# Kernel tuning notes

Measured on AMD Instinct MI355X. Metric: run time of the kernel, lower is better.

The kernel has to match this reference:

```python
import jax, jax.numpy as jnp
import numpy as np

MAX_SCALE = 4
EPS = 1e-7        # tf.keras.backend.epsilon()
BN_EPS = 1e-3     # Keras BatchNormalization default epsilon


def setup_inputs() -> dict:
    key = jax.random.key(0)
    k1, = jax.random.split(key, 1)
    B, H, W, C = 16, 224, 224, 32
    x = jax.random.uniform(k1, (B, H, W, C), dtype=jnp.float32)
    gamma = jnp.ones((C,), jnp.float32)
    beta = jnp.zeros((C,), jnp.float32)
    moving_mean = jnp.zeros((C,), jnp.float32)
    moving_var = jnp.ones((C,), jnp.float32)
    return {"x": x, "gamma": gamma, "beta": beta,
            "moving_mean": moving_mean, "moving_var": moving_var}


def _box_sum(x, r):
    # Depthwise conv with an all-ones (r, r) kernel, SAME padding (NHWC).
    # reduce_window SAME padding matches TF conv SAME for stride 1.
    return jax.lax.reduce_window(x, 0.0, jax.lax.add,
                                 window_dimensions=(1, r, r, 1),
                                 window_strides=(1, 1, 1, 1),
                                 padding="SAME")


def reference(x, gamma, beta, moving_mean, moving_var):
    # sample_min_max_scaling: per-sample min-max over H, W, C
    mn = jnp.min(x, axis=(1, 2, 3), keepdims=True)
    mx = jnp.max(x, axis=(1, 2, 3), keepdims=True)
    xs = (x - mn) / (mx - mn + EPS)

    scales = [2 ** i for i in range(1, MAX_SCALE + 1)]  # [2,4,8,16]
    # measures: [B, H, W, C, S]
    measures = jnp.stack([_box_sum(xs, r) for r in scales], axis=-1)

    # OLS slope of log(measure) vs log(scale), per pixel/channel
    log_scales = jnp.log(jnp.asarray(scales, jnp.float32))        # [S]
    log_measures = jnp.log(measures + EPS)                         # [B,H,W,C,S]
    ls_c = log_scales - jnp.mean(log_scales)                       # centered [S]
    lm_c = log_measures - jnp.mean(log_measures, axis=-1, keepdims=True)
    alphas = jnp.sum(lm_c * ls_c, axis=-1) / jnp.sum(ls_c ** 2)    # [B,H,W,C]

    # BatchNorm, inference mode (training=False)
    inv = jax.lax.rsqrt(moving_var + BN_EPS)
    return (alphas - moving_mean) * inv * gamma + beta
```

## Files before the change

### kernel.cpp

```cpp
#include <hip/hip_runtime.h>
#include <cstdint>

#define B_ 16
#define H_ 224
#define W_ 224
#define C_ 32
#define HW_ (H_*W_)

__device__ __forceinline__ unsigned int enc_f32(float f) {
    unsigned int u = __float_as_uint(f);
    return (u & 0x80000000u) ? ~u : (u | 0x80000000u);
}
__device__ __forceinline__ float dec_f32(unsigned int u) {
    unsigned int v = (u & 0x80000000u) ? (u & 0x7fffffffu) : ~u;
    return __uint_as_float(v);
}

__global__ void k_init(unsigned int* scratch) {
    int t = threadIdx.x;
    if (t < B_) { scratch[t] = 0xFFFFFFFFu; scratch[B_ + t] = 0u; }
}

__global__ __launch_bounds__(256) void k_minmax(
        const float* __restrict__ x, unsigned int* __restrict__ scratch) {
    __shared__ float rmin[4], rmax[4];
    int t = threadIdx.x;
    int b = blockIdx.y;
    const float4* p = (const float4*)(x + (size_t)b * HW_ * C_);
    const int n4 = HW_ * C_ / 4;
    float vmin = 1e30f, vmax = -1e30f;
    for (int i = blockIdx.x * 256 + t; i < n4; i += gridDim.x * 256) {
        float4 v = p[i];
        vmin = fminf(vmin, fminf(fminf(v.x, v.y), fminf(v.z, v.w)));
        vmax = fmaxf(vmax, fmaxf(fmaxf(v.x, v.y), fmaxf(v.z, v.w)));
    }
    for (int off = 32; off; off >>= 1) {
        vmin = fminf(vmin, __shfl_down(vmin, off));
        vmax = fmaxf(vmax, __shfl_down(vmax, off));
    }
    if ((t & 63) == 0) { rmin[t >> 6] = vmin; rmax[t >> 6] = vmax; }
    __syncthreads();
    if (t == 0) {
        atomicMin(&scratch[b],      enc_f32(fminf(fminf(rmin[0], rmin[1]), fminf(rmin[2], rmin[3]))));
        atomicMax(&scratch[B_ + b], enc_f32(fmaxf(fmaxf(rmax[0], rmax[1]), fmaxf(rmax[2], rmax[3]))));
    }
}

__global__ __launch_bounds__(1024, 4) void k_fused(
        const float* __restrict__ x, float* __restrict__ out,
        const float* __restrict__ gamma, const float* __restrict__ beta,
        const float* __restrict__ mmean, const float* __restrict__ mvar,
        const unsigned int* __restrict__ scratch) {
    __shared__ float lin[2][16][132];
    __shared__ float lout[2][16][132];
    const int t    = threadIdx.x;
    const int wid  = t >> 6;
    const int lane = t & 63;

    int bid   = blockIdx.x;
    int cg    = bid & 1;
    int strip = (bid >> 1) & 1;
    int chunk = (bid >> 2) & 3;
    int b     = bid >> 4;

    const int cbase = cg * 16;
    const int c     = cbase + wid;
    const int h0    = chunk * 56;
    const int sbase = strip * 112;

    float sc = gamma[c] * rsqrtf(mvar[c] + 1e-3f);
    float bi = beta[c] - mmean[c] * sc;

    float mn   = dec_f32(scratch[b]);
    float mx   = dec_f32(scratch[B_ + b]);
    float inv  = 1.0f / (mx - mn + 1e-7f);
    float minv = mn * inv;

    int c0 = sbase - 8 + 2 * lane;
    int c1 = c0 + 1;
    bool mC = (c0 >= 0) && (c0 <= W_ - 2);

    int col_l = t >> 3;
    int lch   = (t & 7) * 2;
    int wld   = min(max(sbase - 8 + col_l, 0), W_ - 1);
    int wst   = sbase - 8 + col_l;
    bool colok = (col_l >= 8) && (col_l < 120);
    const float* xb = x   + (size_t)b * HW_ * C_ + cbase + lch;
    float*       ob = out + (size_t)b * HW_ * C_ + cbase + lch;

    float cw2_0  = (float)(min(c0+1, W_-1) - c0 + 1);
    float cw2_1  = (float)(min(c1+1, W_-1) - c1 + 1);
    float cw4_0  = (float)(min(c0+2, W_-1) - max(c0-1, 0) + 1);
    float cw4_1  = (float)(min(c1+2, W_-1) - max(c1-1, 0) + 1);
    float cw8_0  = (float)(min(c0+4, W_-1) - max(c0-3, 0) + 1);
    float cw8_1  = (float)(min(c1+4, W_-1) - max(c1-3, 0) + 1);
    float cw16_0 = (float)(min(c0+8, W_-1) - max(c0-7, 0) + 1);
    float cw16_1 = (float)(min(c1+8, W_-1) - max(c1-7, 0) + 1);
    float e2_0  = minv * cw2_0,  e2_1  = minv * cw2_1;
    float e4_0  = minv * cw4_0,  e4_1  = minv * cw4_1;
    float e8_0  = minv * cw8_0,  e8_1  = minv * cw8_1;
    float e16_0 = minv * cw16_0, e16_1 = minv * cw16_1;
    float d2_0  = 1e-7f -  2.0f * e2_0,  d2_1  = 1e-7f -  2.0f * e2_1;
    float d4_0  = 1e-7f -  4.0f * e4_0,  d4_1  = 1e-7f -  4.0f * e4_1;
    float d8_0  = 1e-7f -  8.0f * e8_0,  d8_1  = 1e-7f -  8.0f * e8_1;
    float d16_0 = 1e-7f - 16.0f * e16_0, d16_1 = 1e-7f - 16.0f * e16_1;

    float hp0 = 0.f, hp1 = 0.f;
    float rB4[2][2]  = {};
    float rB8[2][4]  = {};
    float rB16[2][8] = {};
    float acc[2][8]  = {};

#define LDROW(AR) (*(const float2*)(xb + (size_t)((min(max((AR), 0), H_-1)) * W_ + wld) * C_))

    float2 q0, q1;
    {
        float2 qi = LDROW(h0 - 7);
        lin[1][lch][col_l]     = qi.x;
        lin[1][lch + 1][col_l] = qi.y;
        q0 = LDROW(h0 - 6);
        q1 = LDROW(h0 - 5);
    }

    for (int g8 = 0; g8 < 9; ++g8) {
        #pragma unroll
        for (int u = 0; u < 8; ++u) {
            int it = g8 * 8 + u;
            int a  = h0 - 7 + it;
            __syncthreads();
            float2 lv = *(const float2*)&lin[(u + 1) & 1][wid][2 * lane];
            lin[u & 1][lch][col_l]     = q0.x;
            lin[u & 1][lch + 1][col_l] = q0.y;
            q0 = q1;
            q1 = LDROW(a + 3);
            if (it >= 16 && colok) {
                int op = h0 - 16 + it;
                float2 sv;
                sv.x = lout[u & 1][lch][col_l];
                sv.y = lout[u & 1][lch + 1][col_l];
                *(float2*)(ob + (size_t)(op * W_ + wst) * C_) = sv;
            }

            bool rowok = (a >= 0) && (a < H_);
            float x0 = (rowok && mC) ? lv.x : 0.f;
            float x1 = (rowok && mC) ? lv.y : 0.f;
            float nx0 = __shfl_down(x0, 1);
            float xh0 = x0 + x1;
            float xh1 = x1 + nx0;
            float g2_0 = hp0 + xh0; hp0 = xh0;
            float g2_1 = hp1 + xh1; hp1 = xh1;
            float b4n_0 = g2_0 + __shfl_down(g2_0, 1);
            float b4n_1 = g2_1 + __shfl_down(g2_1, 1);
            float a4_0 = rB4[0][u & 1] + b4n_0; rB4[0][u & 1] = b4n_0;
            float a4_1 = rB4[1][u & 1] + b4n_1; rB4[1][u & 1] = b4n_1;
            float b8n_0 = a4_0 + __shfl_down(a4_0, 2);
            float b8n_1 = a4_1 + __shfl_down(a4_1, 2);
            float a8_0 = rB8[0][u & 3] + b8n_0; rB8[0][u & 3] = b8n_0;
            float a8_1 = rB8[1][u & 3] + b8n_1; rB8[1][u & 3] = b8n_1;
            float b16n_0 = a8_0 + __shfl_down(a8_0, 4);
            float b16n_1 = a8_1 + __shfl_down(a8_1, 4);
            float a16_0 = rB16[0][u] + b16n_0; rB16[0][u] = b16n_0;
            float a16_1 = rB16[1][u] + b16n_1; rB16[1][u] = b16n_1;
            float g4_0  = __shfl_up(a4_1, 1);
            float g4_1  = a4_0;
            float g8_0  = __shfl_up(a8_1, 2);
            float g8_1  = __shfl_up(a8_0, 1);
            float g16_0 = __shfl_up(a16_1, 4);
            float g16_1 = __shfl_up(a16_0, 3);

            float l1_0, l1_1, l2_0, l2_1, l3_0, l3_1, l4_0, l4_1;
            if (a >= 15 && a <= 223) {
                l1_0 = __log2f(fmaxf(fmaf(g2_0,  inv, d2_0 ), 1e-7f));
                l1_1 = __log2f(fmaxf(fmaf(g2_1,  inv, d2_1 ), 1e-7f));
                l2_0 = __log2f(fmaxf(fmaf(g4_0,  inv, d4_0 ), 1e-7f));
                l2_1 = __log2f(fmaxf(fmaf(g4_1,  inv, d4_1 ), 1e-7f));
                l3_0 = __log2f(fmaxf(fmaf(g8_0,  inv, d8_0 ), 1e-7f));
                l3_1 = __log2f(fmaxf(fmaf(g8_1,  inv, d8_1 ), 1e-7f));
                l4_0 = __log2f(fmaxf(fmaf(g16_0, inv, d16_0), 1e-7f));
                l4_1 = __log2f(fmaxf(fmaf(g16_1, inv, d16_1), 1e-7f));
            } else {
                int o1 = a - 1, o2 = a - 2, o3 = a - 4, o4 = a - 8;
                float ch2  = (float)(min(o1+1, H_-1) - o1 + 1);
                float ch4  = (float)(min(o2+2, H_-1) - max(o2-1, 0) + 1);
                float ch8  = (float)(min(o3+4, H_-1) - max(o3-3, 0) + 1);
                float ch16 = (float)(min(o4+8, H_-1) - max(o4-7, 0) + 1);
                l1_0 = __log2f(fmaxf(fmaf(-e2_0,  ch2,  fmaf(g2_0,  inv, 1e-7f)), 1e-7f));
                l1_1 = __log2f(fmaxf(fmaf(-e2_1,  ch2,  fmaf(g2_1,  inv, 1e-7f)), 1e-7f));
                l2_0 = __log2f(fmaxf(fmaf(-e4_0,  ch4,  fmaf(g4_0,  inv, 1e-7f)), 1e-7f));
                l2_1 = __log2f(fmaxf(fmaf(-e4_1,  ch4,  fmaf(g4_1,  inv, 1e-7f)), 1e-7f));
                l3_0 = __log2f(fmaxf(fmaf(-e8_0,  ch8,  fmaf(g8_0,  inv, 1e-7f)), 1e-7f));
                l3_1 = __log2f(fmaxf(fmaf(-e8_1,  ch8,  fmaf(g8_1,  inv, 1e-7f)), 1e-7f));
                l4_0 = __log2f(fmaxf(fmaf(-e16_0, ch16, fmaf(g16_0, inv, 1e-7f)), 1e-7f));
                l4_1 = __log2f(fmaxf(fmaf(-e16_1, ch16, fmaf(g16_1, inv, 1e-7f)), 1e-7f));
            }
            acc[0][u] = -0.3f * l1_0;
            acc[1][u] = -0.3f * l1_1;
            acc[0][(u+7)&7] = fmaf(-0.1f, l2_0, acc[0][(u+7)&7]);
            acc[1][(u+7)&7] = fmaf(-0.1f, l2_1, acc[1][(u+7)&7]);
            acc[0][(u+5)&7] = fmaf( 0.1f, l3_0, acc[0][(u+5)&7]);
            acc[1][(u+5)&7] = fmaf( 0.1f, l3_1, acc[1][(u+5)&7]);
            if (it >= 15 && it <= 70) {
                float al0 = fmaf(0.3f, l4_0, acc[(0)][(u+1)&7]);
                float al1 = fmaf(0.3f, l4_1, acc[(1)][(u+1)&7]);
                float2 ev;
                ev.x = fmaf(sc, al0, bi);
                ev.y = fmaf(sc, al1, bi);
                *(float2*)&lout[(u + 1) & 1][wid][2 * lane] = ev;
            }
        }
    }
#undef LDROW
}

extern "C" void kernel_launch(void* const* d_in, const int* in_sizes, int n_in,
                              void* d_out, int out_size, void* d_ws, size_t ws_size,
                              hipStream_t stream) {
    const float* x     = (const float*)d_in[0];
    const float* gamma = (const float*)d_in[1];
    const float* beta  = (const float*)d_in[2];
    const float* mmean = (const float*)d_in[3];
    const float* mvar  = (const float*)d_in[4];
    float* out = (float*)d_out;

    unsigned int* scratch = (unsigned int*)d_ws;

    k_init<<<1, 64, 0, stream>>>(scratch);
    k_minmax<<<dim3(128, B_), 256, 0, stream>>>(x, scratch);
    k_fused<<<256, 1024, 0, stream>>>(x, out, gamma, beta, mmean, mvar, scratch);
}
```

Measured before the change: 276.0 us.

## Process two rows per barrier with four-deep LDS ring and remapped block order

Widens the shared input/output staging to four row buffers so each barrier covers two row steps, halving the number of __syncthreads in the sliding-window loop. The loads are issued two rows ahead, and output staging is trimmed to valid lanes, which shrinks LDS use. Blocks are remapped so channel group is the outermost index, changing which blocks run together and their cache locality. The price is more live registers, a final-row epilogue, and more complex buffer indexing.

New measurement: 262.5 us. 1.05x faster.

```diff
diff --git a/kernel.cpp b/kernel.cpp
--- a/kernel.cpp
+++ b/kernel.cpp
@@ -51,17 +51,18 @@
         const float* __restrict__ gamma, const float* __restrict__ beta,
         const float* __restrict__ mmean, const float* __restrict__ mvar,
         const unsigned int* __restrict__ scratch) {
-    __shared__ float lin[2][16][132];
-    __shared__ float lout[2][16][132];
+    __shared__ float lin[4][16][130];
+    __shared__ float lout[4][16][116];
     const int t    = threadIdx.x;
     const int wid  = t >> 6;
     const int lane = t & 63;
 
     int bid   = blockIdx.x;
-    int cg    = bid & 1;
-    int strip = (bid >> 1) & 1;
-    int chunk = (bid >> 2) & 3;
-    int b     = bid >> 4;
+    int cg    = bid >> 7;
+    int r     = bid & 127;
+    int strip = r & 1;
+    int chunk = (r >> 1) & 3;
+    int b     = r >> 3;
 
     const int cbase = cg * 16;
     const int c     = cbase + wid;
@@ -79,11 +80,13 @@
     int c0 = sbase - 8 + 2 * lane;
     int c1 = c0 + 1;
     bool mC = (c0 >= 0) && (c0 <= W_ - 2);
+    bool laneok = (lane >= 4) && (lane <= 59);
 
     int col_l = t >> 3;
     int lch   = (t & 7) * 2;
     int wld   = min(max(sbase - 8 + col_l, 0), W_ - 1);
     int wst   = sbase - 8 + col_l;
+    int cs    = col_l - 8;
     bool colok = (col_l >= 8) && (col_l < 120);
     const float* xb = x   + (size_t)b * HW_ * C_ + cbase + lch;
     float*       ob = out + (size_t)b * HW_ * C_ + cbase + lch;
@@ -113,102 +116,125 @@
 
 #define LDROW(AR) (*(const float2*)(xb + (size_t)((min(max((AR), 0), H_-1)) * W_ + wld) * C_))
 
+#define STEP(U_, IT_, A_) do {                                               \
+    float2 lv = *(const float2*)&lin[(U_)&3][wid][2*lane];                   \
+    bool rowok = ((A_) >= 0) && ((A_) < H_);                                 \
+    float x0 = (rowok && mC) ? lv.x : 0.f;                                   \
+    float x1 = (rowok && mC) ? lv.y : 0.f;                                   \
+    float nx0 = __shfl_down(x0, 1);                                          \
+    float xh0 = x0 + x1;                                                     \
+    float xh1 = x1 + nx0;                                                    \
+    float g2_0 = hp0 + xh0; hp0 = xh0;                                       \
+    float g2_1 = hp1 + xh1; hp1 = xh1;                                       \
+    float b4n_0 = g2_0 + __shfl_down(g2_0, 1);                               \
+    float b4n_1 = g2_1 + __shfl_down(g2_1, 1);                               \
+    float a4_0 = rB4[0][(U_)&1] + b4n_0; rB4[0][(U_)&1] = b4n_0;             \
+    float a4_1 = rB4[1][(U_)&1] + b4n_1; rB4[1][(U_)&1] = b4n_1;             \
+    float b8n_0 = a4_0 + __shfl_down(a4_0, 2);                               \
+    float b8n_1 = a4_1 + __shfl_down(a4_1, 2);                               \
+    float a8_0 = rB8[0][(U_)&3] + b8n_0; rB8[0][(U_)&3] = b8n_0;             \
+    float a8_1 = rB8[1][(U_)&3] + b8n_1; rB8[1][(U_)&3] = b8n_1;             \
+    float b16n_0 = a8_0 + __shfl_down(a8_0, 4);                              \
+    float b16n_1 = a8_1 + __shfl_down(a8_1, 4);                              \
+    float a16_0 = rB16[0][(U_)&7] + b16n_0; rB16[0][(U_)&7] = b16n_0;        \
+    float a16_1 = rB16[1][(U_)&7] + b16n_1; rB16[1][(U_)&7] = b16n_1;        \
+    float g4_0  = __shfl_up(a4_1, 1);                                        \
+    float g4_1  = a4_0;                                                      \
+    float g8_0  = __shfl_up(a8_1, 2);                                        \
+    float g8_1  = __shfl_up(a8_0, 1);                                        \
+    float g16_0 = __shfl_up(a16_1, 4);                                       \
+    float g16_1 = __shfl_up(a16_0, 3);                                       \
+    float l1_0, l1_1, l2_0, l2_1, l3_0, l3_1, l4_0, l4_1;                    \
+    if ((A_) >= 15 && (A_) <= 223) {                                         \
+        l1_0 = __log2f(fmaxf(fmaf(g2_0,  inv, d2_0 ), 1e-7f));               \
+        l1_1 = __log2f(fmaxf(fmaf(g2_1,  inv, d2_1 ), 1e-7f));               \
+        l2_0 = __log2f(fmaxf(fmaf(g4_0,  inv, d4_0 ), 1e-7f));               \
+        l2_1 = __log2f(fmaxf(fmaf(g4_1,  inv, d4_1 ), 1e-7f));               \
+        l3_0 = __log2f(fmaxf(fmaf(g8_0,  inv, d8_0 ), 1e-7f));               \
+        l3_1 = __log2f(fmaxf(fmaf(g8_1,  inv, d8_1 ), 1e-7f));               \
+        l4_0 = __log2f(fmaxf(fmaf(g16_0, inv, d16_0), 1e-7f));               \
+        l4_1 = __log2f(fmaxf(fmaf(g16_1, inv, d16_1), 1e-7f));               \
+    } else {                                                                 \
+        int o1 = (A_) - 1, o2 = (A_) - 2, o3 = (A_) - 4, o4 = (A_) - 8;      \
+        float ch2  = (float)(min(o1+1, H_-1) - o1 + 1);                      \
+        float ch4  = (float)(min(o2+2, H_-1) - max(o2-1, 0) + 1);            \
+        float ch8  = (float)(min(o3+4, H_-1) - max(o3-3, 0) + 1);            \
+        float ch16 = (float)(min(o4+8, H_-1) - max(o4-7, 0) + 1);            \
+        l1_0 = __log2f(fmaxf(fmaf(-e2_0,  ch2,  fmaf(g2_0,  inv, 1e-7f)), 1e-7f)); \
+        l1_1 = __log2f(fmaxf(fmaf(-e2_1,  ch2,  fmaf(g2_1,  inv, 1e-7f)), 1e-7f)); \
+        l2_0 = __log2f(fmaxf(fmaf(-e4_0,  ch4,  fmaf(g4_0,  inv, 1e-7f)), 1e-7f)); \
+        l2_1 = __log2f(fmaxf(fmaf(-e4_1,  ch4,  fmaf(g4_1,  inv, 1e-7f)), 1e-7f)); \
+        l3_0 = __log2f(fmaxf(fmaf(-e8_0,  ch8,  fmaf(g8_0,  inv, 1e-7f)), 1e-7f)); \
+        l3_1 = __log2f(fmaxf(fmaf(-e8_1,  ch8,  fmaf(g8_1,  inv, 1e-7f)), 1e-7f)); \
+        l4_0 = __log2f(fmaxf(fmaf(-e16_0, ch16, fmaf(g16_0, inv, 1e-7f)), 1e-7f)); \
+        l4_1 = __log2f(fmaxf(fmaf(-e16_1, ch16, fmaf(g16_1, inv, 1e-7f)), 1e-7f)); \
+    }                                                                        \
+    acc[0][(U_)&7] = -0.3f * l1_0;                                           \
+    acc[1][(U_)&7] = -0.3f * l1_1;                                           \
+    acc[0][((U_)+7)&7] = fmaf(-0.1f, l2_0, acc[0][((U_)+7)&7]);              \
+    acc[1][((U_)+7)&7] = fmaf(-0.1f, l2_1, acc[1][((U_)+7)&7]);              \
+    acc[0][((U_)+5)&7] = fmaf( 0.1f, l3_0, acc[0][((U_)+5)&7]);              \
+    acc[1][((U_)+5)&7] = fmaf( 0.1f, l3_1, acc[1][((U_)+5)&7]);              \
+    if ((IT_) >= 15 && (IT_) <= 70) {                                        \
+        float al0 = fmaf(0.3f, l4_0, acc[0][((U_)+1)&7]);                    \
+        float al1 = fmaf(0.3f, l4_1, acc[1][((U_)+1)&7]);                    \
+        if (laneok) {                                                        \
+            float2 ev;                                                       \
+            ev.x = fmaf(sc, al0, bi);                                        \
+            ev.y = fmaf(sc, al1, bi);                                        \
+            *(float2*)&lout[(U_)&3][wid][2*lane - 8] = ev;                   \
+        }                                                                    \
+    }                                                                        \
+} while (0)
+
     float2 q0, q1;
     {
-        float2 qi = LDROW(h0 - 7);
-        lin[1][lch][col_l]     = qi.x;
-        lin[1][lch + 1][col_l] = qi.y;
-        q0 = LDROW(h0 - 6);
-        q1 = LDROW(h0 - 5);
+        float2 r0 = LDROW(h0 - 7);
+        lin[0][lch][col_l] = r0.x; lin[0][lch + 1][col_l] = r0.y;
+        float2 r1 = LDROW(h0 - 6);
+        lin[1][lch][col_l] = r1.x; lin[1][lch + 1][col_l] = r1.y;
+        q0 = LDROW(h0 - 5);
+        q1 = LDROW(h0 - 4);
     }
 
     for (int g8 = 0; g8 < 9; ++g8) {
         #pragma unroll
-        for (int u = 0; u < 8; ++u) {
-            int it = g8 * 8 + u;
+        for (int ue = 0; ue < 8; ue += 2) {
+            int it = g8 * 8 + ue;
             int a  = h0 - 7 + it;
             __syncthreads();
-            float2 lv = *(const float2*)&lin[(u + 1) & 1][wid][2 * lane];
-            lin[u & 1][lch][col_l]     = q0.x;
-            lin[u & 1][lch + 1][col_l] = q0.y;
-            q0 = q1;
-            q1 = LDROW(a + 3);
+            if (it >= 18 && colok) {
+                int o = h0 - 17 + it;
+                float2 sv;
+                sv.x = lout[(ue + 2) & 3][lch][cs];
+                sv.y = lout[(ue + 2) & 3][lch + 1][cs];
+                *(float2*)(ob + (size_t)(o * W_ + wst) * C_) = sv;
+            }
             if (it >= 16 && colok) {
-                int op = h0 - 16 + it;
+                int o = h0 - 16 + it;
                 float2 sv;
-                sv.x = lout[u & 1][lch][col_l];
-                sv.y = lout[u & 1][lch + 1][col_l];
-                *(float2*)(ob + (size_t)(op * W_ + wst) * C_) = sv;
+                sv.x = lout[(ue + 3) & 3][lch][cs];
+                sv.y = lout[(ue + 3) & 3][lch + 1][cs];
+                *(float2*)(ob + (size_t)(o * W_ + wst) * C_) = sv;
             }
-
-            bool rowok = (a >= 0) && (a < H_);
-            float x0 = (rowok && mC) ? lv.x : 0.f;
-            float x1 = (rowok && mC) ? lv.y : 0.f;
-            float nx0 = __shfl_down(x0, 1);
-            float xh0 = x0 + x1;
-            float xh1 = x1 + nx0;
-            float g2_0 = hp0 + xh0; hp0 = xh0;
-            float g2_1 = hp1 + xh1; hp1 = xh1;
-            float b4n_0 = g2_0 + __shfl_down(g2_0, 1);
-            float b4n_1 = g2_1 + __shfl_down(g2_1, 1);
-            float a4_0 = rB4[0][u & 1] + b4n_0; rB4[0][u & 1] = b4n_0;
-            float a4_1 = rB4[1][u & 1] + b4n_1; rB4[1][u & 1] = b4n_1;
-            float b8n_0 = a4_0 + __shfl_down(a4_0, 2);
-            float b8n_1 = a4_1 + __shfl_down(a4_1, 2);
-            float a8_0 = rB8[0][u & 3] + b8n_0; rB8[0][u & 3] = b8n_0;
-            float a8_1 = rB8[1][u & 3] + b8n_1; rB8[1][u & 3] = b8n_1;
-            float b16n_0 = a8_0 + __shfl_down(a8_0, 4);
-            float b16n_1 = a8_1 + __shfl_down(a8_1, 4);
-            float a16_0 = rB16[0][u] + b16n_0; rB16[0][u] = b16n_0;
-            float a16_1 = rB16[1][u] + b16n_1; rB16[1][u] = b16n_1;
-            float g4_0  = __shfl_up(a4_1, 1);
-            float g4_1  = a4_0;
-            float g8_0  = __shfl_up(a8_1, 2);
-            float g8_1  = __shfl_up(a8_0, 1);
-            float g16_0 = __shfl_up(a16_1, 4);
-            float g16_1 = __shfl_up(a16_0, 3);
-
-            float l1_0, l1_1, l2_0, l2_1, l3_0, l3_1, l4_0, l4_1;
-            if (a >= 15 && a <= 223) {
-                l1_0 = __log2f(fmaxf(fmaf(g2_0,  inv, d2_0 ), 1e-7f));
-                l1_1 = __log2f(fmaxf(fmaf(g2_1,  inv, d2_1 ), 1e-7f));
-                l2_0 = __log2f(fmaxf(fmaf(g4_0,  inv, d4_0 ), 1e-7f));
-                l2_1 = __log2f(fmaxf(fmaf(g4_1,  inv, d4_1 ), 1e-7f));
-                l3_0 = __log2f(fmaxf(fmaf(g8_0,  inv, d8_0 ), 1e-7f));
-                l3_1 = __log2f(fmaxf(fmaf(g8_1,  inv, d8_1 ), 1e-7f));
-                l4_0 = __log2f(fmaxf(fmaf(g16_0, inv, d16_0), 1e-7f));
-                l4_1 = __log2f(fmaxf(fmaf(g16_1, inv, d16_1), 1e-7f));
-            } else {
-                int o1 = a - 1, o2 = a - 2, o3 = a - 4, o4 = a - 8;
-                float ch2  = (float)(min(o1+1, H_-1) - o1 + 1);
-                float ch4  = (float)(min(o2+2, H_-1) - max(o2-1, 0) + 1);
-                float ch8  = (float)(min(o3+4, H_-1) - max(o3-3, 0) + 1);
-                float ch16 = (float)(min(o4+8, H_-1) - max(o4-7, 0) + 1);
-                l1_0 = __log2f(fmaxf(fmaf(-e2_0,  ch2,  fmaf(g2_0,  inv, 1e-7f)), 1e-7f));
-                l1_1 = __log2f(fmaxf(fmaf(-e2_1,  ch2,  fmaf(g2_1,  inv, 1e-7f)), 1e-7f));
-                l2_0 = __log2f(fmaxf(fmaf(-e4_0,  ch4,  fmaf(g4_0,  inv, 1e-7f)), 1e-7f));
-                l2_1 = __log2f(fmaxf(fmaf(-e4_1,  ch4,  fmaf(g4_1,  inv, 1e-7f)), 1e-7f));
-                l3_0 = __log2f(fmaxf(fmaf(-e8_0,  ch8,  fmaf(g8_0,  inv, 1e-7f)), 1e-7f));
-                l3_1 = __log2f(fmaxf(fmaf(-e8_1,  ch8,  fmaf(g8_1,  inv, 1e-7f)), 1e-7f));
-                l4_0 = __log2f(fmaxf(fmaf(-e16_0, ch16, fmaf(g16_0, inv, 1e-7f)), 1e-7f));
-                l4_1 = __log2f(fmaxf(fmaf(-e16_1, ch16, fmaf(g16_1, inv, 1e-7f)), 1e-7f));
-            }
-            acc[0][u] = -0.3f * l1_0;
-            acc[1][u] = -0.3f * l1_1;
-            acc[0][(u+7)&7] = fmaf(-0.1f, l2_0, acc[0][(u+7)&7]);
-            acc[1][(u+7)&7] = fmaf(-0.1f, l2_1, acc[1][(u+7)&7]);
-            acc[0][(u+5)&7] = fmaf( 0.1f, l3_0, acc[0][(u+5)&7]);
-            acc[1][(u+5)&7] = fmaf( 0.1f, l3_1, acc[1][(u+5)&7]);
-            if (it >= 15 && it <= 70) {
-                float al0 = fmaf(0.3f, l4_0, acc[(0)][(u+1)&7]);
-                float al1 = fmaf(0.3f, l4_1, acc[(1)][(u+1)&7]);
-                float2 ev;
-                ev.x = fmaf(sc, al0, bi);
-                ev.y = fmaf(sc, al1, bi);
-                *(float2*)&lout[(u + 1) & 1][wid][2 * lane] = ev;
-            }
+            lin[(ue + 2) & 3][lch][col_l]     = q0.x;
+            lin[(ue + 2) & 3][lch + 1][col_l] = q0.y;
+            lin[(ue + 3) & 3][lch][col_l]     = q1.x;
+            lin[(ue + 3) & 3][lch + 1][col_l] = q1.y;
+            q0 = LDROW(a + 4);
+            q1 = LDROW(a + 5);
+            STEP(ue,     it,     a);
+            STEP(ue + 1, it + 1, a + 1);
         }
     }
+    __syncthreads();
+    if (colok) {
+        float2 sv;
+        sv.x = lout[2][lch][cs];
+        sv.y = lout[2][lch + 1][cs];
+        *(float2*)(ob + (size_t)((h0 + 55) * W_ + wst) * C_) = sv;
+    }
+#undef STEP
 #undef LDROW
 }
 
```
